# Performance work log

Measured on AMD Instinct MI355X. Metric: run time of the kernel, lower is better.

## Reference

```python
import jax, jax.numpy as jnp
import numpy as np

TRANSLATE_STD = 0.125
SCALE_STD = 0.2
CUTOUT_SIZE = 0.5

B, C, H, W = 64, 3, 512, 512


def setup_inputs() -> dict:
    key = jax.random.key(0)
    ks = jax.random.split(key, 20)
    inp = {
        'images': jax.random.normal(ks[0], (B, C, H, W), dtype=jnp.float32),
        'u_angle': jax.random.uniform(ks[1], (B,), dtype=jnp.float32),
        'u_scale': jax.random.uniform(ks[2], (B,), dtype=jnp.float32),
        'u_trans': jax.random.uniform(ks[3], (B,), dtype=jnp.float32),
        'u_bright': jax.random.uniform(ks[4], (B,), dtype=jnp.float32),
        'u_contrast': jax.random.uniform(ks[5], (B,), dtype=jnp.float32),
        'u_sat': jax.random.uniform(ks[6], (B,), dtype=jnp.float32),
        'noise': jax.random.normal(ks[7], (B, C, H, W), dtype=jnp.float32),
        'm_flip': jax.random.randint(ks[8], (B,), 0, 2, dtype=jnp.int32),
        'm_rot': jax.random.randint(ks[9], (B,), 0, 2, dtype=jnp.int32),
        'm_scale': jax.random.randint(ks[10], (B,), 0, 2, dtype=jnp.int32),
        'm_trans': jax.random.randint(ks[11], (B,), 0, 2, dtype=jnp.int32),
        'm_bright': jax.random.randint(ks[12], (B,), 0, 2, dtype=jnp.int32),
        'm_contrast': jax.random.randint(ks[13], (B,), 0, 2, dtype=jnp.int32),
        'm_sat': jax.random.randint(ks[14], (B,), 0, 2, dtype=jnp.int32),
        'm_cut': jax.random.randint(ks[15], (B,), 0, 2, dtype=jnp.int32),
        'y0': jax.random.randint(ks[16], (B,), 0, H - int(H * CUTOUT_SIZE) + 1, dtype=jnp.int32),
        'x0': jax.random.randint(ks[17], (B,), 0, W - int(W * CUTOUT_SIZE) + 1, dtype=jnp.int32),
    }
    return inp


def _sample_bilinear_reflect(img, gx, gy):
    # img: [C,H,W]; gx, gy: [H,W] normalized coords in grid_sample convention
    # (align_corners=False, padding_mode='reflection')
    c, h, w = img.shape
    x = ((gx + 1.0) * w - 1.0) * 0.5
    y = ((gy + 1.0) * h - 1.0) * 0.5

    def reflect(v, size):
        # reflect about pixel edges [-0.5, size-0.5], then clip coordinate
        v = jnp.abs(v + 0.5)
        v = jnp.mod(v, 2.0 * size)
        v = jnp.minimum(v, 2.0 * size - v)
        return jnp.clip(v - 0.5, 0.0, size - 1.0)

    x = reflect(x, float(w))
    y = reflect(y, float(h))
    x0f = jnp.floor(x)
    y0f = jnp.floor(y)
    wx = x - x0f
    wy = y - y0f
    x0i = jnp.clip(x0f, 0, w - 1).astype(jnp.int32)
    x1i = jnp.clip(x0f + 1, 0, w - 1).astype(jnp.int32)
    y0i = jnp.clip(y0f, 0, h - 1).astype(jnp.int32)
    y1i = jnp.clip(y0f + 1, 0, h - 1).astype(jnp.int32)
    v00 = img[:, y0i, x0i]
    v01 = img[:, y0i, x1i]
    v10 = img[:, y1i, x0i]
    v11 = img[:, y1i, x1i]
    top = v00 + wx * (v01 - v00)
    bot = v10 + wx * (v11 - v10)
    return top + wy * (bot - top)


def reference(images, u_angle, u_scale, u_trans, u_bright, u_contrast, u_sat,
              noise, m_flip, m_rot, m_scale, m_trans, m_bright, m_contrast,
              m_sat, m_cut, y0, x0):
    b, c, h, w = images.shape
    # xflip
    images = jnp.where((m_flip > 0)[:, None, None, None], images[..., ::-1], images)
    # rotate / scale / translate (single value broadcast to both axes, as in original)
    angle = jnp.where(m_rot > 0, (u_angle * 2.0 - 1.0) * jnp.pi, 0.0)
    sc = jnp.where(m_scale > 0, (u_scale * 2.0 - 1.0) * SCALE_STD + 1.0, 1.0)
    tr = jnp.where(m_trans > 0, (u_trans * 2.0 - 1.0) * TRANSLATE_STD, 0.0)
    ca = jnp.cos(angle)[:, None, None]
    sa = jnp.sin(angle)[:, None, None]
    scb = sc[:, None, None]
    trb = tr[:, None, None]
    gx0, gy0 = jnp.meshgrid(jnp.linspace(-1.0, 1.0, w), jnp.linspace(-1.0, 1.0, h), indexing='xy')  # [H,W]
    gx = scb * (ca * gx0 - sa * gy0) + trb  # [B,H,W]
    gy = scb * (sa * gx0 + ca * gy0) + trb
    images = jax.vmap(_sample_bilinear_reflect)(images, gx, gy)
    # brightness
    bb = jnp.where(m_bright > 0, u_bright * 0.2, 0.0)
    images = jnp.clip(images + bb[:, None, None, None], -1.0, 1.0)
    # contrast
    cc = jnp.where(m_contrast > 0, u_contrast + 0.5, 1.0)
    images = jnp.clip(images * cc[:, None, None, None], -1.0, 1.0)
    # saturation: lerp(grayscale, images, s)
    ss = jnp.where(m_sat > 0, u_sat * 2.0, 1.0)[:, None, None, None]
    gray = images.mean(axis=1, keepdims=True)
    images = jnp.clip(gray + ss * (images - gray), -1.0, 1.0)
    ch, cw = int(h * CUTOUT_SIZE), int(w * CUTOUT_SIZE)
    ys = jnp.arange(h)[None, :, None]
    xs = jnp.arange(w)[None, None, :]
    y0b = y0[:, None, None]
    x0b = x0[:, None, None]
    cmask = (ys >= y0b) & (ys < y0b + ch) & (xs >= x0b) & (xs < x0b + cw)
    fmask = cmask & (m_cut > 0)[:, None, None]
    images = jnp.where(fmask[:, None, :, :], noise, images)
    return images
```

## Files before the change

### kernel.cpp

```cpp
#include <hip/hip_runtime.h>
#include <math.h>


constexpr int Bn = 64;
constexpr int Cn = 3;
constexpr int Hn = 512;
constexpr int Wn = 512;
constexpr float TRANSLATE_STD = 0.125f;
constexpr float SCALE_STD = 0.2f;
constexpr int CUT_H = 256;
constexpr int CUT_W = 256;

constexpr int FW = 32;
constexpr int FSTRIDE = 40;
constexpr int FH_MAX = 32;
constexpr int CH_LDS = FSTRIDE * FH_MAX;
constexpr int NT = 8;
constexpr uint32_t PLANE = 512u * 512u;

typedef float f4v __attribute__((ext_vector_type(4)));
typedef float f2v __attribute__((ext_vector_type(2)));

__device__ __forceinline__ f2v load2(const float* p) {
    f2v r;
    __builtin_memcpy(&r, p, 8);
    return r;
}

__device__ __forceinline__ float reflect_coord(float v, float size) {
    v = fabsf(v + 0.5f);
    v = fmodf(v, 2.0f * size);
    v = fminf(v, 2.0f * size - v);
    return fminf(fmaxf(v - 0.5f, 0.0f), size - 1.0f);
}

__global__ __launch_bounds__(256) void augment_kernel(
    const float* __restrict__ images,
    const float* __restrict__ u_angle,
    const float* __restrict__ u_scale,
    const float* __restrict__ u_trans,
    const float* __restrict__ u_bright,
    const float* __restrict__ u_contrast,
    const float* __restrict__ u_sat,
    const float* __restrict__ noise,
    const int* __restrict__ m_flip,
    const int* __restrict__ m_rot,
    const int* __restrict__ m_scale,
    const int* __restrict__ m_trans,
    const int* __restrict__ m_bright,
    const int* __restrict__ m_contrast,
    const int* __restrict__ m_sat,
    const int* __restrict__ m_cut,
    const int* __restrict__ y0p,
    const int* __restrict__ x0p,
    float* __restrict__ out)
{
    __shared__ __align__(16) float lds[Cn * CH_LDS];

    const int tx  = threadIdx.x;
    const int ty  = threadIdx.y;
    const int sx0 = blockIdx.x * (16 * NT);
    const int y   = blockIdx.y * 16 + ty;
    const int b   = blockIdx.z;

    const float angle = (m_rot[b] > 0) ? (u_angle[b] * 2.0f - 1.0f) * 3.14159265358979323846f : 0.0f;
    const float sc    = (m_scale[b] > 0) ? (u_scale[b] * 2.0f - 1.0f) * SCALE_STD + 1.0f : 1.0f;
    const float tr    = (m_trans[b] > 0) ? (u_trans[b] * 2.0f - 1.0f) * TRANSLATE_STD : 0.0f;
    const float bb    = (m_bright[b] > 0) ? u_bright[b] * 0.2f : 0.0f;
    const float cc    = (m_contrast[b] > 0) ? u_contrast[b] + 0.5f : 1.0f;
    const float ss    = (m_sat[b] > 0) ? u_sat[b] * 2.0f : 1.0f;
    const bool  flip  = m_flip[b] > 0;
    const bool  docut = m_cut[b] > 0;
    const int   cy0   = y0p[b];
    const int   cx0   = x0p[b];

    float saf, caf;
    __sincosf(angle, &saf, &caf);

    const float kk = sc * (512.0f / 511.0f);
    const float dxdx = caf * kk, dxdy = -saf * kk;
    const float dydx = saf * kk, dydy = caf * kk;
    const float xx_org = 256.0f * (sc * (saf - caf) + tr + 1.0f) - 0.5f;
    const float yy_org = 256.0f * (sc * (-saf - caf) + tr + 1.0f) - 0.5f;

    const float step_x = 16.0f * dxdx;
    const float step_y = 16.0f * dydx;

    float xxt = xx_org + (float)(sx0 + tx) * dxdx + (float)y * dxdy;
    float yyt = yy_org + (float)(sx0 + tx) * dydx + (float)y * dydy;

    const float fty = (float)(blockIdx.y * 16);
    float bx = xx_org + (float)sx0 * dxdx + fty * dxdy;
    float by = yy_org + (float)sx0 * dydx + fty * dydy;
    const float sxx = 15.0f * dxdx, sxy = 15.0f * dxdy;
    const float syx = 15.0f * dydx, syy = 15.0f * dydy;
    const float min_dx = fminf(sxx, 0.0f) + fminf(sxy, 0.0f);
    const float max_dx = fmaxf(sxx, 0.0f) + fmaxf(sxy, 0.0f);
    const float min_dy = fminf(syx, 0.0f) + fminf(syy, 0.0f);
    const float max_dy = fmaxf(syx, 0.0f) + fmaxf(syy, 0.0f);

    const float* __restrict__ imgb = images + (size_t)b * (Cn * PLANE);
    float* __restrict__ outb       = out    + (size_t)b * (Cn * PLANE);
    const float* __restrict__ noib = noise  + (size_t)b * (Cn * PLANE);

    const int tid = ty * 16 + tx;
    const int sr  = tid >> 3;
    const int sq  = (tid & 7) << 2;

    const bool ycut = docut && (y >= cy0) && (y < cy0 + CUT_H);
    uint32_t opix = (uint32_t)y * 512u + (uint32_t)(sx0 + tx);

    #pragma unroll 1
    for (int t = 0; t < NT; ++t) {
        const float minxx = bx + min_dx, maxxx = bx + max_dx;
        const float minyy = by + min_dy, maxyy = by + max_dy;
        bool cok = (minxx >= 1.0f) && (maxxx <= 509.0f) &&
                   (minyy >= 1.0f) && (maxyy <= 509.0f);
        int x_lo = 0, y_lo = 0, fh = 0;
        if (cok) {
            x_lo = min(((int)minxx - 1) & ~3, Wn - FW);
            y_lo = (int)minyy - 1;
            fh   = ((int)maxyy + 2) - y_lo + 1;
            if (fh > FH_MAX) cok = false;
        }

        if (t > 0) __syncthreads();

        if (cok && sr < fh) {
            const int scol = flip ? (508 - x_lo - sq) : (x_lo + sq);
            const uint32_t soff = (uint32_t)(y_lo + sr) * 512u + (uint32_t)scol;
            f4v A = *(const f4v*)(imgb + soff);
            f4v B = *(const f4v*)(imgb + soff + PLANE);
            f4v C = *(const f4v*)(imgb + soff + 2 * PLANE);
            if (flip) {
                A = f4v{A.w, A.z, A.y, A.x};
                B = f4v{B.w, B.z, B.y, B.x};
                C = f4v{C.w, C.z, C.y, C.x};
            }
            float* d = &lds[sr * FSTRIDE + sq];
            *(f4v*)(d)              = A;
            *(f4v*)(d + CH_LDS)     = B;
            *(f4v*)(d + 2 * CH_LDS) = C;
        }
        __syncthreads();

        float vals[Cn];
        if (cok) {
            const float fx = xxt - (float)x_lo;
            const float fy = yyt - (float)y_lo;
            const int xi = (int)fx;
            const int yi = (int)fy;
            const float wx = fx - (float)xi;
            const float wy = fy - (float)yi;
            const float* ph = &lds[yi * FSTRIDE + xi];
            #pragma unroll
            for (int c = 0; c < Cn; ++c) {
                const float v00 = ph[0], v01 = ph[1];
                const float v10 = ph[FSTRIDE], v11 = ph[FSTRIDE + 1];
                ph += CH_LDS;
                const float top = v00 + wx * (v01 - v00);
                const float bot = v10 + wx * (v11 - v10);
                float v = top + wy * (bot - top);
                v = __builtin_amdgcn_fmed3f(v + bb, -1.0f, 1.0f);
                v = __builtin_amdgcn_fmed3f(v * cc, -1.0f, 1.0f);
                vals[c] = v;
            }
        } else {
            const float rxx = reflect_coord(xxt, (float)Wn);
            const float ryy = reflect_coord(yyt, (float)Hn);
            const float x0f = floorf(rxx);
            const float y0f = floorf(ryy);
            const float wx = rxx - x0f;
            const float wy = ryy - y0f;
            int x0i = (int)fminf(fmaxf(x0f, 0.0f), 511.0f);
            int x1i = (int)fminf(x0f + 1.0f, 511.0f);
            const int y0i = (int)fminf(fmaxf(y0f, 0.0f), 511.0f);
            const int y1i = (int)fminf(y0f + 1.0f, 511.0f);
            if (flip) { x0i = 511 - x0i; x1i = 511 - x1i; }
            const int xbase = min(min(x0i, x1i), 510);
            const bool s0 = (x0i != xbase);
            const bool s1 = (x1i != xbase);
            const uint32_t r0 = (uint32_t)(y0i * 512 + xbase);
            const uint32_t r1 = (uint32_t)(y1i * 512 + xbase);
            #pragma unroll
            for (int c = 0; c < Cn; ++c) {
                const f2v t0 = load2(imgb + r0 + c * PLANE);
                const f2v t1 = load2(imgb + r1 + c * PLANE);
                const float v00 = s0 ? t0.y : t0.x;
                const float v01 = s1 ? t0.y : t0.x;
                const float v10 = s0 ? t1.y : t1.x;
                const float v11 = s1 ? t1.y : t1.x;
                const float top = v00 + wx * (v01 - v00);
                const float bot = v10 + wx * (v11 - v10);
                float v = top + wy * (bot - top);
                v = __builtin_amdgcn_fmed3f(v + bb, -1.0f, 1.0f);
                v = __builtin_amdgcn_fmed3f(v * cc, -1.0f, 1.0f);
                vals[c] = v;
            }
        }

        const float gray = (vals[0] + vals[1] + vals[2]) * (1.0f / 3.0f);
        const int xpix = sx0 + (t << 4) + tx;
        const bool cut = ycut && (xpix >= cx0) && (xpix < cx0 + CUT_W);
        #pragma unroll
        for (int c = 0; c < Cn; ++c) {
            float v = gray + ss * (vals[c] - gray);
            v = __builtin_amdgcn_fmed3f(v, -1.0f, 1.0f);
            if (cut) v = __builtin_nontemporal_load(&noib[opix + c * PLANE]);
            __builtin_nontemporal_store(v, &outb[opix + c * PLANE]);
        }

        opix += 16;
        bx += step_x; by += step_y;
        xxt += step_x; yyt += step_y;
    }
}

extern "C" void kernel_launch(void* const* d_in, const int* in_sizes, int n_in,
                              void* d_out, int out_size, void* d_ws, size_t ws_size,
                              hipStream_t stream) {
    const float* images     = (const float*)d_in[0];
    const float* u_angle    = (const float*)d_in[1];
    const float* u_scale    = (const float*)d_in[2];
    const float* u_trans    = (const float*)d_in[3];
    const float* u_bright   = (const float*)d_in[4];
    const float* u_contrast = (const float*)d_in[5];
    const float* u_sat      = (const float*)d_in[6];
    const float* noise      = (const float*)d_in[7];
    const int*   m_flip     = (const int*)d_in[8];
    const int*   m_rot      = (const int*)d_in[9];
    const int*   m_scale    = (const int*)d_in[10];
    const int*   m_trans    = (const int*)d_in[11];
    const int*   m_bright   = (const int*)d_in[12];
    const int*   m_contrast = (const int*)d_in[13];
    const int*   m_sat      = (const int*)d_in[14];
    const int*   m_cut      = (const int*)d_in[15];
    const int*   y0p        = (const int*)d_in[16];
    const int*   x0p        = (const int*)d_in[17];
    float* out = (float*)d_out;

    dim3 block(16, 16);
    dim3 grid(Wn / (16 * NT), Hn / 16, Bn);
    augment_kernel<<<grid, block, 0, stream>>>(
        images, u_angle, u_scale, u_trans, u_bright, u_contrast, u_sat, noise,
        m_flip, m_rot, m_scale, m_trans, m_bright, m_contrast, m_sat, m_cut,
        y0p, x0p, out);
}
```

Before: 517.8 us.

## Prefetch next tile's source rows into registers and swizzle block order

Restructures the tile loop so the global loads for the next sub-tile are issued into registers before the current sub-tile is computed, then written to LDS after a barrier. This is a register-staged software pipeline that hides global load latency. It also remaps the linear block index with a swizzle so consecutively scheduled blocks spread across batches and rows, which changes cache and channel locality. The cost is extra registers and an additional barrier per iteration.

```diff
diff --git a/kernel.cpp b/kernel.cpp
--- a/kernel.cpp
+++ b/kernel.cpp
@@ -32,6 +32,12 @@
     v = fmodf(v, 2.0f * size);
     v = fminf(v, 2.0f * size - v);
     return fminf(fmaxf(v - 0.5f, 0.0f), size - 1.0f);
+}
+
+__device__ __forceinline__ void pipe_barrier() {
+    asm volatile("s_waitcnt lgkmcnt(0)" ::: "memory");
+    __builtin_amdgcn_s_barrier();
+    __builtin_amdgcn_sched_barrier(0);
 }
 
 __global__ __launch_bounds__(256) void augment_kernel(
@@ -57,11 +63,15 @@
 {
     __shared__ __align__(16) float lds[Cn * CH_LDS];
 
+    const int lin = blockIdx.x + (blockIdx.y << 2) + (blockIdx.z << 7);
+    const int swz = ((lin & 7) << 10) + (lin >> 3);
+    const int sx0 = (swz & 3) << 7;
+    const int y16 = (swz >> 2) & 31;
+    const int b   = swz >> 7;
+
     const int tx  = threadIdx.x;
     const int ty  = threadIdx.y;
-    const int sx0 = blockIdx.x * (16 * NT);
-    const int y   = blockIdx.y * 16 + ty;
-    const int b   = blockIdx.z;
+    const int y   = (y16 << 4) + ty;
 
     const float angle = (m_rot[b] > 0) ? (u_angle[b] * 2.0f - 1.0f) * 3.14159265358979323846f : 0.0f;
     const float sc    = (m_scale[b] > 0) ? (u_scale[b] * 2.0f - 1.0f) * SCALE_STD + 1.0f : 1.0f;
@@ -89,7 +99,7 @@
     float xxt = xx_org + (float)(sx0 + tx) * dxdx + (float)y * dxdy;
     float yyt = yy_org + (float)(sx0 + tx) * dydx + (float)y * dydy;
 
-    const float fty = (float)(blockIdx.y * 16);
+    const float fty = (float)(y16 << 4);
     float bx = xx_org + (float)sx0 * dxdx + fty * dxdy;
     float by = yy_org + (float)sx0 * dydx + fty * dydy;
     const float sxx = 15.0f * dxdx, sxy = 15.0f * dxdy;
@@ -110,44 +120,56 @@
     const bool ycut = docut && (y >= cy0) && (y < cy0 + CUT_H);
     uint32_t opix = (uint32_t)y * 512u + (uint32_t)(sx0 + tx);
 
-    #pragma unroll 1
-    for (int t = 0; t < NT; ++t) {
-        const float minxx = bx + min_dx, maxxx = bx + max_dx;
-        const float minyy = by + min_dy, maxyy = by + max_dy;
-        bool cok = (minxx >= 1.0f) && (maxxx <= 509.0f) &&
-                   (minyy >= 1.0f) && (maxyy <= 509.0f);
-        int x_lo = 0, y_lo = 0, fh = 0;
-        if (cok) {
+    int cx_lo, cy_lo, cfh; bool cok;
+    int nx_lo, ny_lo, nfh; bool nok;
+    auto mkbox = [&](float bxv, float byv, int& x_lo, int& y_lo, int& fh, bool& ok) {
+        const float minxx = bxv + min_dx, maxxx = bxv + max_dx;
+        const float minyy = byv + min_dy, maxyy = byv + max_dy;
+        ok = (minxx >= 1.0f) && (maxxx <= 509.0f) &&
+             (minyy >= 1.0f) && (maxyy <= 509.0f);
+        x_lo = 0; y_lo = 0; fh = 0;
+        if (ok) {
             x_lo = min(((int)minxx - 1) & ~3, Wn - FW);
             y_lo = (int)minyy - 1;
             fh   = ((int)maxyy + 2) - y_lo + 1;
-            if (fh > FH_MAX) cok = false;
-        }
-
-        if (t > 0) __syncthreads();
-
-        if (cok && sr < fh) {
-            const int scol = flip ? (508 - x_lo - sq) : (x_lo + sq);
-            const uint32_t soff = (uint32_t)(y_lo + sr) * 512u + (uint32_t)scol;
-            f4v A = *(const f4v*)(imgb + soff);
-            f4v B = *(const f4v*)(imgb + soff + PLANE);
-            f4v C = *(const f4v*)(imgb + soff + 2 * PLANE);
-            if (flip) {
-                A = f4v{A.w, A.z, A.y, A.x};
-                B = f4v{B.w, B.z, B.y, B.x};
-                C = f4v{C.w, C.z, C.y, C.x};
-            }
-            float* d = &lds[sr * FSTRIDE + sq];
-            *(f4v*)(d)              = A;
-            *(f4v*)(d + CH_LDS)     = B;
-            *(f4v*)(d + 2 * CH_LDS) = C;
-        }
-        __syncthreads();
-
+            if (fh > FH_MAX) ok = false;
+        }
+    };
+
+    f4v A{}, B{}, C{};
+    auto loadR = [&](int x_lo, int y_lo) {
+        const int scol = flip ? (508 - x_lo - sq) : (x_lo + sq);
+        const uint32_t soff = (uint32_t)(y_lo + sr) * 512u + (uint32_t)scol;
+        A = *(const f4v*)(imgb + soff);
+        B = *(const f4v*)(imgb + soff + PLANE);
+        C = *(const f4v*)(imgb + soff + 2 * PLANE);
+    };
+    auto writeR = [&]() {
+        f4v a = A, b2 = B, c2 = C;
+        if (flip) {
+            a  = f4v{A.w, A.z, A.y, A.x};
+            b2 = f4v{B.w, B.z, B.y, B.x};
+            c2 = f4v{C.w, C.z, C.y, C.x};
+        }
+        float* d = &lds[sr * FSTRIDE + sq];
+        *(f4v*)(d)              = a;
+        *(f4v*)(d + CH_LDS)     = b2;
+        *(f4v*)(d + 2 * CH_LDS) = c2;
+    };
+
+    mkbox(bx, by, cx_lo, cy_lo, cfh, cok);
+    if (cok && sr < cfh) { loadR(cx_lo, cy_lo); writeR(); }
+    bx += step_x; by += step_y;
+    mkbox(bx, by, nx_lo, ny_lo, nfh, nok);
+    if (nok && sr < nfh) loadR(nx_lo, ny_lo);
+    pipe_barrier();
+
+    #pragma unroll 1
+    for (int t = 0; t < NT; ++t) {
         float vals[Cn];
         if (cok) {
-            const float fx = xxt - (float)x_lo;
-            const float fy = yyt - (float)y_lo;
+            const float fx = xxt - (float)cx_lo;
+            const float fy = yyt - (float)cy_lo;
             const int xi = (int)fx;
             const int yi = (int)fy;
             const float wx = fx - (float)xi;
@@ -209,10 +231,22 @@
             if (cut) v = __builtin_nontemporal_load(&noib[opix + c * PLANE]);
             __builtin_nontemporal_store(v, &outb[opix + c * PLANE]);
         }
-
         opix += 16;
+        xxt += step_x; yyt += step_y;
+
+        if (t == NT - 1) break;
+
+        pipe_barrier();
+        cx_lo = nx_lo; cy_lo = ny_lo; cfh = nfh; cok = nok;
+        if (cok && sr < cfh) writeR();
         bx += step_x; by += step_y;
-        xxt += step_x; yyt += step_y;
+        if (t + 2 < NT) {
+            mkbox(bx, by, nx_lo, ny_lo, nfh, nok);
+            if (nok && sr < nfh) loadR(nx_lo, ny_lo);
+        } else {
+            nok = false;
+        }
+        pipe_barrier();
     }
 }
 
```

Measured after the change: 509.5 us. Within noise of the previous version (-1.6%).
